# Kernel tuning notes

Hardware: AMD Instinct MI355X
Metric: run time of the kernel (lower is better)

## Reference

```python
import jax, jax.numpy as jnp
import numpy as np

CUTOFF = 15.0
EPS = 1e-08


def _pairwise_dist(x):
    # x: [B, N, 3] -> [B, N, N] euclidean distances (gram trick, no [B,N,N,3] temp)
    x2 = jnp.sum(x * x, axis=-1)                      # [B, N]
    d2 = x2[:, :, None] + x2[:, None, :] - 2.0 * jnp.einsum('bnd,bmd->bnm', x, x)
    d2 = jnp.maximum(d2, 0.0)
    return jnp.sqrt(d2)


def setup_inputs() -> dict:
    key = jax.random.key(0)
    k1, k2 = jax.random.split(key)
    B, N = 8, 2048
    pred_coords = jax.random.normal(k1, (B, N, 3), dtype=jnp.float32)
    true_coords = jax.random.normal(k2, (B, N, 3), dtype=jnp.float32)
    return {"pred_coords": pred_coords, "true_coords": true_coords}


def reference(pred_coords, true_coords):
    pred_d = _pairwise_dist(pred_coords)              # [B, N, N]
    true_d = _pairwise_dist(true_coords)              # [B, N, N]
    local_mask = (true_d < CUTOFF) & (true_d > EPS)   # excludes diagonal
    diff = jnp.abs(pred_d - true_d)
    # piecewise-constant preserved score (0.5/1.0/2.0/4.0 A bins)
    preserved = (
        (diff < 0.5).astype(jnp.float32) * 1.0
        + ((diff >= 0.5) & (diff < 1.0)).astype(jnp.float32) * 0.5
        + ((diff >= 1.0) & (diff < 2.0)).astype(jnp.float32) * 0.25
        + ((diff >= 2.0) & (diff < 4.0)).astype(jnp.float32) * 0.125
    )
    maskf = local_mask.astype(jnp.float32)
    numerator = jnp.sum(preserved * maskf, axis=(-1, -2))    # [B]
    denominator = jnp.maximum(jnp.sum(maskf, axis=(-1, -2)), EPS)
    lddt_per_sample = numerator / denominator
    return jnp.mean(1.0 - lddt_per_sample)
```

## Files before the change

kernel.cpp:

```cpp
#include <hip/hip_runtime.h>
#include <math.h>

constexpr int B  = 8;
constexpr int N  = 2048;
constexpr int TI = 64;
constexpr int TJ = 64;
constexpr int TILES = 528;

template <bool CHECK>
__device__ __forceinline__ void inner_loop(
    const float4* __restrict__ sj,
    float pix, float piy, float piz,
    float tix, float tiy, float tiz,
    int j0, int i,
    unsigned& c0, unsigned& c1, unsigned& c2, unsigned& c3, unsigned& cd)
{
    #pragma unroll 8
    for (int j = 0; j < TJ; ++j) {
        float4 p4 = sj[2 * j + 0];
        float4 t4 = sj[2 * j + 1];

        float dx = pix - p4.x, dy = piy - p4.y, dz = piz - p4.z;
        float pd2 = fmaf(dx, dx, fmaf(dy, dy, dz * dz));
        float ex = tix - t4.x, ey = tiy - t4.y, ez = tiz - t4.z;
        float td2 = fmaf(ex, ex, fmaf(ey, ey, ez * ez));

        unsigned long long m = __ballot(td2 < 225.0f);
        if (CHECK) m &= __ballot(j0 + j > i);

        float diff = fabsf(__builtin_amdgcn_sqrtf(pd2) - __builtin_amdgcn_sqrtf(td2));

        c0 += __popcll(m & __ballot(diff < 0.5f));
        c1 += __popcll(m & __ballot(diff < 1.0f));
        c2 += __popcll(m & __ballot(diff < 2.0f));
        c3 += __popcll(m & __ballot(diff < 4.0f));
        cd += __popcll(m);
    }
}

__global__ __launch_bounds__(TI) void lddt_partial(
    const float* __restrict__ pred,
    const float* __restrict__ truec,
    float2* __restrict__ part)
{
    const int b = blockIdx.y;
    int r = blockIdx.x, a = 0;
    while (r >= 32 - a) { r -= 32 - a; ++a; }
    const int c = a + r;
    const int i0 = a * TI;
    const int j0 = c * TJ;
    const int t = threadIdx.x;

    __shared__ float4 sj[TJ * 2];

    const float* pp = pred  + ((size_t)b * N + j0 + t) * 3;
    const float* tp = truec + ((size_t)b * N + j0 + t) * 3;
    sj[2 * t + 0] = make_float4(pp[0], pp[1], pp[2], 0.0f);
    sj[2 * t + 1] = make_float4(tp[0], tp[1], tp[2], 0.0f);

    const int i = i0 + t;
    const float* pi = pred  + ((size_t)b * N + i) * 3;
    const float* ti = truec + ((size_t)b * N + i) * 3;
    const float pix = pi[0], piy = pi[1], piz = pi[2];
    const float tix = ti[0], tiy = ti[1], tiz = ti[2];
    __syncthreads();

    unsigned c0 = 0, c1 = 0, c2 = 0, c3 = 0, cd = 0;

    if (c > a) {
        inner_loop<false>(sj, pix, piy, piz, tix, tiy, tiz, j0, i, c0, c1, c2, c3, cd);
    } else {
        inner_loop<true>(sj, pix, piy, piz, tix, tiy, tiz, j0, i, c0, c1, c2, c3, cd);
    }

    if (t == 0) {
        float n = 0.5f * (float)c0 + 0.25f * (float)c1
                + 0.125f * (float)c2 + 0.125f * (float)c3;
        part[(size_t)b * TILES + blockIdx.x] = make_float2(n, (float)cd);
    }
}

__global__ __launch_bounds__(512) void lddt_reduce(
    const float2* __restrict__ part,
    float* __restrict__ out)
{
    const int t = threadIdx.x;
    const int w = t >> 6;
    const int l = t & 63;

    float n = 0.0f, d = 0.0f;
    for (int s = l; s < TILES; s += 64) {
        float2 v = part[(size_t)w * TILES + s];
        n += v.x;
        d += v.y;
    }
    for (int off = 32; off > 0; off >>= 1) {
        n += __shfl_down(n, off, 64);
        d += __shfl_down(d, off, 64);
    }

    __shared__ float acc[B];
    if (l == 0) acc[w] = 1.0f - n / fmaxf(d, 1e-8f);
    __syncthreads();

    if (t == 0) {
        float s = 0.0f;
        #pragma unroll
        for (int b = 0; b < B; ++b) s += acc[b];
        out[0] = s / (float)B;
    }
}

extern "C" void kernel_launch(void* const* d_in, const int* in_sizes, int n_in,
                              void* d_out, int out_size, void* d_ws, size_t ws_size,
                              hipStream_t stream)
{
    const float* pred  = (const float*)d_in[0];
    const float* truec = (const float*)d_in[1];
    float* out   = (float*)d_out;
    float2* part = (float2*)d_ws;

    dim3 grid(TILES, B);
    lddt_partial<<<grid, TI, 0, stream>>>(pred, truec, part);
    lddt_reduce<<<1, 512, 0, stream>>>(part, out);
}
```

Measured before the change: 73.43 us.

## Use 256-thread blocks with wave-uniform global j loads and bitmask diagonal test

Each block now covers 256 i rows against 64 j columns, as four waves, with the upper-triangle tile enumeration rewritten to match. The shared-memory staging and the barrier are gone. Each wave reads the j coordinates straight from global memory at wave-uniform addresses, so they can become scalar loads. The diagonal mask is built from a lane bitmask instead of a ballot, and each wave writes its own partial sum. The aim is to cut LDS traffic, synchronisation and block-launch overhead, at the cost of some wasted wave work in diagonal tiles and fewer, larger blocks.

```diff
diff --git a/kernel.cpp b/kernel.cpp
--- a/kernel.cpp
+++ b/kernel.cpp
@@ -3,30 +3,37 @@
 
 constexpr int B  = 8;
 constexpr int N  = 2048;
-constexpr int TI = 64;
+constexpr int TI = 256;
 constexpr int TJ = 64;
-constexpr int TILES = 528;
+constexpr int TILES = 144;
+constexpr int WPB = TI / 64;
 
 template <bool CHECK>
 __device__ __forceinline__ void inner_loop(
-    const float4* __restrict__ sj,
+    const float* __restrict__ pj,
+    const float* __restrict__ tj,
     float pix, float piy, float piz,
     float tix, float tiy, float tiz,
-    int j0, int i,
+    int k0,
     unsigned& c0, unsigned& c1, unsigned& c2, unsigned& c3, unsigned& cd)
 {
-    #pragma unroll 8
+    #pragma unroll 4
     for (int j = 0; j < TJ; ++j) {
-        float4 p4 = sj[2 * j + 0];
-        float4 t4 = sj[2 * j + 1];
+        float pjx = pj[3 * j + 0], pjy = pj[3 * j + 1], pjz = pj[3 * j + 2];
+        float tjx = tj[3 * j + 0], tjy = tj[3 * j + 1], tjz = tj[3 * j + 2];
 
-        float dx = pix - p4.x, dy = piy - p4.y, dz = piz - p4.z;
+        float dx = pix - pjx, dy = piy - pjy, dz = piz - pjz;
         float pd2 = fmaf(dx, dx, fmaf(dy, dy, dz * dz));
-        float ex = tix - t4.x, ey = tiy - t4.y, ez = tiz - t4.z;
+        float ex = tix - tjx, ey = tiy - tjy, ez = tiz - tjz;
         float td2 = fmaf(ex, ex, fmaf(ey, ey, ez * ez));
 
         unsigned long long m = __ballot(td2 < 225.0f);
-        if (CHECK) m &= __ballot(j0 + j > i);
+        if (CHECK) {
+            int kw = k0 + j;
+            unsigned long long mji =
+                (kw >= 64) ? ~0ull : ((kw <= 0) ? 0ull : ((1ull << kw) - 1ull));
+            m &= mji;
+        }
 
         float diff = fabsf(__builtin_amdgcn_sqrtf(pd2) - __builtin_amdgcn_sqrtf(td2));
 
@@ -45,38 +52,38 @@
 {
     const int b = blockIdx.y;
     int r = blockIdx.x, a = 0;
-    while (r >= 32 - a) { r -= 32 - a; ++a; }
-    const int c = a + r;
+    while (r >= 32 - 4 * a) { r -= 32 - 4 * a; ++a; }
+    const int c = 4 * a + r;
     const int i0 = a * TI;
     const int j0 = c * TJ;
     const int t = threadIdx.x;
-
-    __shared__ float4 sj[TJ * 2];
-
-    const float* pp = pred  + ((size_t)b * N + j0 + t) * 3;
-    const float* tp = truec + ((size_t)b * N + j0 + t) * 3;
-    sj[2 * t + 0] = make_float4(pp[0], pp[1], pp[2], 0.0f);
-    sj[2 * t + 1] = make_float4(tp[0], tp[1], tp[2], 0.0f);
+    const int wave = t >> 6;
 
     const int i = i0 + t;
     const float* pi = pred  + ((size_t)b * N + i) * 3;
     const float* ti = truec + ((size_t)b * N + i) * 3;
     const float pix = pi[0], piy = pi[1], piz = pi[2];
     const float tix = ti[0], tiy = ti[1], tiz = ti[2];
-    __syncthreads();
+
+    const float* pj = pred  + ((size_t)b * N + j0) * 3;
+    const float* tj = truec + ((size_t)b * N + j0) * 3;
 
     unsigned c0 = 0, c1 = 0, c2 = 0, c3 = 0, cd = 0;
 
-    if (c > a) {
-        inner_loop<false>(sj, pix, piy, piz, tix, tiy, tiz, j0, i, c0, c1, c2, c3, cd);
+    if (c >= 4 * a + 4) {
+        inner_loop<false>(pj, tj, pix, piy, piz, tix, tiy, tiz, 0,
+                          c0, c1, c2, c3, cd);
     } else {
-        inner_loop<true>(sj, pix, piy, piz, tix, tiy, tiz, j0, i, c0, c1, c2, c3, cd);
+        const int k0 = j0 - (i0 + 64 * wave);
+        inner_loop<true>(pj, tj, pix, piy, piz, tix, tiy, tiz, k0,
+                         c0, c1, c2, c3, cd);
     }
 
-    if (t == 0) {
+    if ((t & 63) == 0) {
         float n = 0.5f * (float)c0 + 0.25f * (float)c1
                 + 0.125f * (float)c2 + 0.125f * (float)c3;
-        part[(size_t)b * TILES + blockIdx.x] = make_float2(n, (float)cd);
+        part[(size_t)b * (TILES * WPB) + blockIdx.x * WPB + wave] =
+            make_float2(n, (float)cd);
     }
 }
 
@@ -84,13 +91,14 @@
     const float2* __restrict__ part,
     float* __restrict__ out)
 {
+    constexpr int SLOTS = TILES * WPB;
     const int t = threadIdx.x;
     const int w = t >> 6;
     const int l = t & 63;
 
     float n = 0.0f, d = 0.0f;
-    for (int s = l; s < TILES; s += 64) {
-        float2 v = part[(size_t)w * TILES + s];
+    for (int s = l; s < SLOTS; s += 64) {
+        float2 v = part[(size_t)w * SLOTS + s];
         n += v.x;
         d += v.y;
     }
```

New measurement: 76.84 us. 1.05x slower.
